# Performance work log

Hardware: AMD Instinct MI355X
Metric: run time of the kernel (lower is better)

The kernel has to match this reference:

```python
import jax, jax.numpy as jnp
from jax import lax
import numpy as np

B, T, H, W = 8, 32, 128, 128
D_MODEL, D_STATE, D_CONV, EXPAND = 256, 16, 4, 2
D_INNER = EXPAND * D_MODEL
DT_RANK = 16  # ceil(d_model/16)
CHANS = [3, 32, 64, 96]
COV_SCALE = 0.01


def setup_inputs() -> dict:
    key = jax.random.key(0)
    ks = iter(jax.random.split(key, 64))
    def n(shape, s=0.02):
        return jax.random.normal(next(ks), shape, dtype=jnp.float32) * s
    inp = {
        "frames": jax.random.normal(next(ks), (B, T, 3, H, W), dtype=jnp.float32),
        "target_bboxes": jax.random.uniform(next(ks), (B, T, 4), dtype=jnp.float32),
    }
    for i in range(3):
        inp[f"conv_w{i}"] = n((CHANS[i + 1], CHANS[i], 3, 3, 3))
        inp[f"conv_b{i}"] = jnp.zeros((CHANS[i + 1],), jnp.float32)
        inp[f"bn_g{i}"] = jnp.ones((CHANS[i + 1],), jnp.float32)
        inp[f"bn_b{i}"] = jnp.zeros((CHANS[i + 1],), jnp.float32)
    inp["ep_w"] = n((D_MODEL, CHANS[-1])); inp["ep_b"] = jnp.zeros((D_MODEL,), jnp.float32)
    inp["bp1_w"] = n((64, 4), 0.1); inp["bp1_b"] = jnp.zeros((64,), jnp.float32)
    inp["bp2_w"] = n((D_MODEL, 64)); inp["bp2_b"] = jnp.zeros((D_MODEL,), jnp.float32)
    inp["in_proj_w"] = n((2 * D_INNER, D_MODEL))
    inp["conv1d_w"] = n((D_INNER, 1, D_CONV), 0.1)
    inp["conv1d_b"] = jnp.zeros((D_INNER,), jnp.float32)
    inp["x_proj_w"] = n((DT_RANK + 2 * D_STATE, D_INNER))
    inp["dt_proj_w"] = n((D_INNER, DT_RANK), 0.1)
    inp["dt_proj_b"] = jnp.full((D_INNER,), -3.0, jnp.float32)
    inp["A_log"] = jnp.log(jnp.broadcast_to(jnp.arange(1, D_STATE + 1, dtype=jnp.float32), (D_INNER, D_STATE)))
    inp["D_param"] = jnp.ones((D_INNER,), jnp.float32)
    inp["out_proj_w"] = n((D_MODEL, D_INNER))
    inp["h1_w"] = n((D_MODEL // 2, D_MODEL)); inp["h1_b"] = jnp.zeros((D_MODEL // 2,), jnp.float32)
    inp["h2_w"] = n((4, D_MODEL // 2), 0.1); inp["h2_b"] = jnp.zeros((4,), jnp.float32)
    inp["kf_F"] = jnp.eye(4, dtype=jnp.float32) + n((4, 4), 0.01)
    inp["kf_H"] = jnp.eye(4, dtype=jnp.float32) + n((4, 4), 0.01)
    inp["kf_log_q"] = n((4,), 1.0) - 2.0
    inp["kf_log_r"] = n((4,), 1.0) - 2.0
    return inp


DN3D = ("NCDHW", "OIDHW", "NCDHW")


def _forward(frames, target_bboxes, conv_w0, conv_b0, bn_g0, bn_b0,
             conv_w1, conv_b1, bn_g1, bn_b1, conv_w2, conv_b2, bn_g2, bn_b2,
             ep_w, ep_b, bp1_w, bp1_b, bp2_w, bp2_b,
             in_proj_w, conv1d_w, conv1d_b, x_proj_w, dt_proj_w, dt_proj_b,
             A_log, D_param, out_proj_w, h1_w, h1_b, h2_w, h2_b,
             kf_F, kf_H, kf_log_q, kf_log_r):
    Bn, Tn = frames.shape[0], frames.shape[1]

    # ---- bbox_proj: Linear(4,64) -> ReLU -> Linear(64,d_model) ----
    bf = jax.nn.relu(target_bboxes @ bp1_w.T + bp1_b) @ bp2_w.T + bp2_b  # (B,T,Dm)

    # ---- 3D conv encoder (BN in eval mode: running stats 0/1 -> affine only) ----
    x = jnp.transpose(frames, (0, 2, 1, 3, 4))  # (B,C,T,H,W)
    for (w, b, g, be) in ((conv_w0, conv_b0, bn_g0, bn_b0),
                          (conv_w1, conv_b1, bn_g1, bn_b1),
                          (conv_w2, conv_b2, bn_g2, bn_b2)):
        x = lax.conv_general_dilated(x, w, (1, 2, 2), ((1, 1), (1, 1), (1, 1)),
                                     dimension_numbers=DN3D) + b[None, :, None, None, None]
        x = g[None, :, None, None, None] * x + be[None, :, None, None, None]
        x = jax.nn.relu(x)
        x = lax.reduce_window(x, -jnp.inf, lax.max, (1, 1, 1, 2, 2), (1, 1, 1, 2, 2), "VALID")
    x = x.mean(axis=(3, 4))                    # AdaptiveAvgPool3d((None,1,1)) -> (B,Cenc,T)
    ff = jnp.transpose(x, (0, 2, 1)) @ ep_w.T + ep_b  # (B,T,Dm)

    u = ff + bf

    # ---- Mamba block ----
    xz = u @ in_proj_w.T                        # (B,T,2*Di)
    xm, z = jnp.split(xz, 2, axis=-1)
    xc = jnp.transpose(xm, (0, 2, 1))           # (B,Di,T)
    xc = lax.conv_general_dilated(xc, conv1d_w, (1,), ((D_CONV - 1, 0),),
                                  dimension_numbers=("NCW", "OIW", "NCW"),
                                  feature_group_count=D_INNER) + conv1d_b[None, :, None]
    xs = jax.nn.silu(jnp.transpose(xc, (0, 2, 1)))  # (B,T,Di)
    xdbl = xs @ x_proj_w.T
    dt, Bm, Cm = jnp.split(xdbl, [DT_RANK, DT_RANK + D_STATE], axis=-1)
    dt = jax.nn.softplus(dt @ dt_proj_w.T + dt_proj_b)    # (B,T,Di)
    A = -jnp.exp(A_log)                                    # (Di,Ds)
    dA = jnp.exp(dt[..., None] * A)                        # (B,T,Di,Ds)
    dBx = dt[..., None] * Bm[:, :, None, :] * xs[..., None]

    def ssm_step(h, inputs):
        dA_t, dBx_t, C_t = inputs
        h = dA_t * h + dBx_t                               # (B,Di,Ds)
        y = jnp.einsum("bds,bs->bd", h, C_t)
        return h, y

    h0 = jnp.zeros((Bn, D_INNER, D_STATE), xs.dtype)
    _, ys = lax.scan(ssm_step, h0, (jnp.transpose(dA, (1, 0, 2, 3)),
                                    jnp.transpose(dBx, (1, 0, 2, 3)),
                                    jnp.transpose(Cm, (1, 0, 2))))
    y = jnp.transpose(ys, (1, 0, 2)) + D_param * xs
    y = y * jax.nn.silu(z)
    mo = y @ out_proj_w.T                                  # (B,T,Dm)

    # ---- measurement head ----
    meas = jax.nn.sigmoid(jax.nn.relu(mo @ h1_w.T + h1_b) @ h2_w.T + h2_b)  # (B,T,4)

    # ---- Kalman filter over T (scan) ----
    Q = jnp.diag(jnp.exp(kf_log_q) + 1e-6)
    R = jnp.diag(jnp.exp(kf_log_r) + 1e-6)
    I4 = jnp.eye(4, dtype=meas.dtype)
    Hb = jnp.broadcast_to(kf_H, (Bn, 4, 4))

    def kf_step(carry, m_t):
        s, P = carry
        s_pred = jnp.einsum("ij,bjk->bik", kf_F, s)
        P_pred = jnp.einsum("ij,bjk,lk->bil", kf_F, P, kf_F) + Q
        yres = m_t - jnp.einsum("ij,bjk->bik", kf_H, s_pred)
        S = jnp.einsum("ij,bjk,lk->bil", kf_H, P_pred, kf_H) + R
        SinvH = jnp.linalg.solve(S, Hb)                    # S^{-1} H
        K = jnp.einsum("bij,bkj->bik", P_pred, SinvH)      # P H^T S^{-T}
        s_new = s_pred + K @ yres
        IKH = I4 - K @ kf_H
        P_new = IKH @ P_pred @ jnp.swapaxes(IKH, -1, -2) + (K @ R) @ jnp.swapaxes(K, -1, -2)
        return (s_new, P_new), s_new[..., 0]

    state0 = target_bboxes[:, 0, :, None]                  # (B,4,1)
    cov0 = jnp.broadcast_to(I4 * COV_SCALE, (Bn, 4, 4))
    _, preds = lax.scan(kf_step, (state0, cov0), jnp.transpose(meas, (1, 0, 2))[..., None])
    kf_pred = jnp.transpose(preds, (1, 0, 2))              # (B,T,4)
    return kf_pred, meas


def reference(frames, target_bboxes, conv_w0, conv_b0, bn_g0, bn_b0,
              conv_w1, conv_b1, bn_g1, bn_b1, conv_w2, conv_b2, bn_g2, bn_b2,
              ep_w, ep_b, bp1_w, bp1_b, bp2_w, bp2_b,
              in_proj_w, conv1d_w, conv1d_b, x_proj_w, dt_proj_w, dt_proj_b,
              A_log, D_param, out_proj_w, h1_w, h1_b, h2_w, h2_b,
              kf_F, kf_H, kf_log_q, kf_log_r):
    return _forward(frames, target_bboxes, conv_w0, conv_b0, bn_g0, bn_b0,
                    conv_w1, conv_b1, bn_g1, bn_b1, conv_w2, conv_b2, bn_g2, bn_b2,
                    ep_w, ep_b, bp1_w, bp1_b, bp2_w, bp2_b,
                    in_proj_w, conv1d_w, conv1d_b, x_proj_w, dt_proj_w, dt_proj_b,
                    A_log, D_param, out_proj_w, h1_w, h1_b, h2_w, h2_b,
                    kf_F, kf_H, kf_log_q, kf_log_r)
```

## Files before the change

### kernel.cpp

```cpp
#include <hip/hip_runtime.h>
#include <math.h>

constexpr int Bn = 8, Tn = 32;
constexpr int D_INNER = 512;

typedef __attribute__((ext_vector_type(8))) short short8;
typedef __attribute__((ext_vector_type(8))) unsigned short ushort8;
typedef __attribute__((ext_vector_type(4))) float f32x4;

__device__ inline unsigned short f2bf(float x) {
    unsigned int u = __float_as_uint(x);
    unsigned int r = (u + 0x7FFF + ((u >> 16) & 1)) >> 16;
    return (unsigned short)r;
}

__global__ void prep_all(
    const float* __restrict__ cw0, const float* __restrict__ cw1,
    const float* __restrict__ cw2,
    const float* __restrict__ ip, const float* __restrict__ xp,
    const float* __restrict__ dt, const float* __restrict__ op,
    const float* __restrict__ h1, const float* __restrict__ h2,
    const float* __restrict__ ep, const float* __restrict__ bp2,
    const float* __restrict__ bp1,
    unsigned short* __restrict__ w0b, unsigned short* __restrict__ w1b,
    unsigned short* __restrict__ w2b, float* __restrict__ tW)
{
    int idx = blockIdx.x * blockDim.x + threadIdx.x;
    if (idx < 9216) {
        int d = idx;
        int sl = d & 7, sq = (d >> 3) & 3, co = (d >> 5) & 31;
        int r = d >> 10; int ky = r % 3, kt = r / 3;
        int q = sq ^ (co & 3) ^ ((co >> 2) & 3);
        float v = 0.f;
        if (q < 3 && sl < 3)
            v = cw0[((((size_t)co * 3 + sl) * 3 + kt) * 3 + ky) * 3 + q];
        w0b[d] = f2bf(v);
    } else if (idx < 64512) {
        int d = idx - 9216;
        int sl = d & 7, sg = (d >> 3) & 3, co = (d >> 5) & 63;
        int r = d >> 11; int k9 = r % 9, kt = r / 9;
        int ci = (sg ^ (co & 3)) * 8 + sl;
        w1b[d] = f2bf(cw1[((size_t)(co * 32 + ci) * 3 + kt) * 9 + k9]);
    } else if (idx < 230400) {
        int d = idx - 64512;
        int cip = d & 31; int rest = d >> 5;
        int co = rest % 96; rest /= 96;
        int k9 = rest % 9; int hh = rest / 9;
        int h = hh & 1, kt = hh >> 1;
        int ci = h * 32 + cip;
        w2b[d] = f2bf(cw2[((size_t)(co * 64 + ci) * 3 + kt) * 9 + k9]);
    } else if (idx < 730880) {
        int d = idx - 230400;
        const float* src; int N, K, base;
        if      (d < 262144) { src = ip;  N = 1024; K = 256; base = 0; }
        else if (d < 286720) { src = xp;  N = 48;   K = 512; base = 262144; }
        else if (d < 294912) { src = dt;  N = 512;  K = 16;  base = 286720; }
        else if (d < 425984) { src = op;  N = 256;  K = 512; base = 294912; }
        else if (d < 458752) { src = h1;  N = 128;  K = 256; base = 425984; }
        else if (d < 459264) { src = h2;  N = 4;    K = 128; base = 458752; }
        else if (d < 483840) { src = ep;  N = 256;  K = 96;  base = 459264; }
        else if (d < 500224) { src = bp2; N = 256;  K = 64;  base = 483840; }
        else                 { src = bp1; N = 64;   K = 4;   base = 500224; }
        int s = d - base;
        int o = s / K, k = s - o * K;
        tW[base + k * N + o] = src[s];
    }
}

constexpr int C0_STR  = 68;
constexpr int C0_BLKS = 17 * C0_STR;

__device__ inline void conv0_fill(unsigned short* dst, const float* __restrict__ in,
                                  int b, int ts, int yt, int xh, int tid)
{
    bool tok = (ts >= 0 && ts < Tn);
    const float* src = in + (size_t)(b * Tn + (tok ? ts : 0)) * 3 * 16384;
    for (int e = tid; e < C0_BLKS; e += 512) {
        int r = e / C0_STR, c = e - r * C0_STR;
        int gy = 16 * yt - 1 + r;
        int x  = 64 * xh + c - 1;
        bool ok = tok && gy >= 0 && gy < 128 && x >= 0 && x < 128;
        float v0 = 0.f, v1 = 0.f, v2 = 0.f;
        if (ok) {
            const float* p = src + gy * 128 + x;
            v0 = p[0]; v1 = p[16384]; v2 = p[32768];
        }
        ushort8 pk = (ushort8)0;
        pk[0] = f2bf(v0); pk[1] = f2bf(v1); pk[2] = f2bf(v2);
        *(ushort8*)(dst + (size_t)e * 8) = pk;
    }
}

__global__ __launch_bounds__(512) void conv0_kernel(
    const float* __restrict__ in, const unsigned short* __restrict__ w0b,
    const float* __restrict__ bias, const float* __restrict__ gam,
    const float* __restrict__ bet, unsigned short* __restrict__ out)
{
    int tid  = threadIdx.x;
    int lane = tid & 63;
    int wv   = __builtin_amdgcn_readfirstlane(tid >> 6);
    int q    = lane >> 4;
    int l15  = lane & 15;
    int pyp  = wv >> 1;
    int hx   = wv & 1;
    int bI = blockIdx.x;
    int bt = bI >> 4, yt = (bI >> 1) & 7, xh = bI & 1;
    int b = bt >> 5, t = bt & 31;

    __shared__ __align__(16) unsigned short S[C0_BLKS * 8];
    __shared__ __align__(16) unsigned short W[9 * 32 * 32];

    f32x4 acc[2][2];
    #pragma unroll
    for (int dy = 0; dy < 2; ++dy)
        #pragma unroll
        for (int nt = 0; nt < 2; ++nt) acc[dy][nt] = (f32x4)0.f;

    {
        const uint4* wsrc = (const uint4*)w0b;
        uint4* wdst = (uint4*)W;
        for (int e = tid; e < 1152; e += 512) wdst[e] = wsrc[e];
    }

    int oxl = hx * 16 + l15;

    for (int kt = 0; kt < 3; ++kt) {
        __syncthreads();
        conv0_fill(S, in, b, t + kt - 1, yt, xh, tid);
        __syncthreads();

        #pragma unroll
        for (int ky = 0; ky < 3; ++ky) {
            short8 bfr[2];
            #pragma unroll
            for (int nt = 0; nt < 2; ++nt) {
                int co = nt * 16 + l15;
                int i16 = ((kt * 3 + ky) * 32 + co) * 4 +
                          (q ^ (co & 3) ^ ((co >> 2) & 3));
                bfr[nt] = *(const short8*)(W + (size_t)i16 * 8);
            }
            #pragma unroll
            for (int dy = 0; dy < 2; ++dy) {
                int r = 4 * pyp + 2 * dy + ky;
                short8 af = (short8)0;
                if (q < 3)
                    af = *(const short8*)(S + (size_t)(r * C0_STR + 2 * oxl + q) * 8);
                #pragma unroll
                for (int nt = 0; nt < 2; ++nt)
                    acc[dy][nt] = __builtin_amdgcn_mfma_f32_16x16x32_bf16(
                        af, bfr[nt], acc[dy][nt], 0, 0, 0);
            }
        }
    }

    unsigned short* dst = out + (size_t)bt * 32768;
    #pragma unroll
    for (int nt = 0; nt < 2; ++nt) {
        int co = nt * 16 + l15;
        float bi = bias[co], g = gam[co], be = bet[co];
        #pragma unroll
        for (int j = 0; j < 2; ++j) {
            float m0 = fmaxf(fmaf(g, acc[0][nt][2 * j]     + bi, be), 0.f);
            float m1 = fmaxf(fmaf(g, acc[0][nt][2 * j + 1] + bi, be), 0.f);
            float m2 = fmaxf(fmaf(g, acc[1][nt][2 * j]     + bi, be), 0.f);
            float m3 = fmaxf(fmaf(g, acc[1][nt][2 * j + 1] + bi, be), 0.f);
            float p = fmaxf(fmaxf(m0, m1), fmaxf(m2, m3));
            int pox = xh * 16 + hx * 8 + q * 2 + j;
            int poy = yt * 4 + pyp;
            dst[(poy * 32 + pox) * 32 + co] = f2bf(p);
        }
    }
}

__global__ __launch_bounds__(512) void conv1_kernel(
    const unsigned short* __restrict__ in, const unsigned short* __restrict__ w1b,
    const float* __restrict__ bias, const float* __restrict__ gam,
    const float* __restrict__ bet, unsigned short* __restrict__ out)
{
    int tid  = threadIdx.x;
    int lane = tid & 63;
    int wv   = tid >> 6;
    int q    = lane >> 4;
    int l15  = lane & 15;
    int oyp  = wv >> 1;
    int nh   = wv & 1;
    int bt = blockIdx.x >> 1, half = blockIdx.x & 1;
    int b = bt >> 5, t = bt & 31;

    __shared__ __align__(16) unsigned short S[17 * 34 * 32];
    __shared__ __align__(16) unsigned short W[9 * 64 * 32];

    f32x4 acc[2][2];
    #pragma unroll
    for (int mt = 0; mt < 2; ++mt)
        #pragma unroll
        for (int nt = 0; nt < 2; ++nt) acc[mt][nt] = (f32x4)0.f;

    for (int kt = 0; kt < 3; ++kt) {
        int ts = t + kt - 1;
        if (ts < 0 || ts >= Tn) continue;
        __syncthreads();
        const unsigned short* src = in + (size_t)(b * Tn + ts) * 32768;
        for (int e = tid; e < 17 * 34 * 4; e += 512) {
            int sb = e & 3;
            int pos = e >> 2;
            int ys = pos / 34, xs = pos - ys * 34;
            int g = sb ^ ((xs >> 1) & 3);
            int y = 16 * half + ys - 1, x = xs - 1;
            ushort8 v = (ushort8)0;
            if (y >= 0 && x >= 0 && x < 32)
                v = *(const ushort8*)(src + ((y * 32 + x) * 32 + g * 8));
            *(ushort8*)(S + (size_t)e * 8) = v;
        }
        {
            const uint4* wsrc = (const uint4*)(w1b + kt * 18432);
            uint4* wdst = (uint4*)W;
            for (int e = tid; e < 2304; e += 512) wdst[e] = wsrc[e];
        }
        __syncthreads();

        for (int k9 = 0; k9 < 9; ++k9) {
            int ky = k9 / 3, kx = k9 - ky * 3;
            short8 bf[2];
            #pragma unroll
            for (int nt = 0; nt < 2; ++nt) {
                int co = nh * 32 + nt * 16 + l15;
                int blk = (k9 * 64 + co) * 4 + (q ^ (co & 3));
                bf[nt] = *(const short8*)(W + blk * 8);
            }
            short8 af[2];
            #pragma unroll
            for (int mt = 0; mt < 2; ++mt) {
                int oyl = 2 * oyp + mt;
                int ys = 2 * oyl + ky;
                int xs = 2 * l15 + kx;
                int blk = (ys * 34 + xs) * 4 + (q ^ ((xs >> 1) & 3));
                af[mt] = *(const short8*)(S + blk * 8);
            }
            #pragma unroll
            for (int mt = 0; mt < 2; ++mt)
                #pragma unroll
                for (int nt = 0; nt < 2; ++nt)
                    acc[mt][nt] = __builtin_amdgcn_mfma_f32_16x16x32_bf16(
                        af[mt], bf[nt], acc[mt][nt], 0, 0, 0);
        }
    }

    unsigned short* dst = out + (size_t)bt * 4096;
    #pragma unroll
    for (int nt = 0; nt < 2; ++nt) {
        int co = nh * 32 + nt * 16 + l15;
        float bi = bias[co], g = gam[co], be = bet[co];
        #pragma unroll
        for (int j = 0; j < 2; ++j) {
            float m0 = fmaxf(fmaf(g, acc[0][nt][2 * j]     + bi, be), 0.f);
            float m1 = fmaxf(fmaf(g, acc[0][nt][2 * j + 1] + bi, be), 0.f);
            float m2 = fmaxf(fmaf(g, acc[1][nt][2 * j]     + bi, be), 0.f);
            float m3 = fmaxf(fmaf(g, acc[1][nt][2 * j + 1] + bi, be), 0.f);
            float p = fmaxf(fmaxf(m0, m1), fmaxf(m2, m3));
            int px = 2 * q + j, py = half * 4 + oyp;
            dst[(py * 8 + px) * 64 + co] = f2bf(p);
        }
    }
}

__global__ __launch_bounds__(384) void conv2_kernel(
    const unsigned short* __restrict__ in, const unsigned short* __restrict__ w2b,
    const float* __restrict__ bias, const float* __restrict__ gam,
    const float* __restrict__ bet, float* __restrict__ out)
{
    int tid  = threadIdx.x;
    int lane = tid & 63;
    int wv   = tid >> 6;
    int q    = lane >> 4;
    int l15  = lane & 15;
    int bt = blockIdx.x;
    int b = bt >> 5, t = bt & 31;

    __shared__ __align__(16) unsigned short W[864 * 5 * 8];
    __shared__ __align__(16) unsigned short S[81 * 5 * 8];

    f32x4 acc = (f32x4)0.f;

    for (int kt = 0; kt < 3; ++kt) {
        int ts = t + kt - 1;
        if (ts < 0 || ts >= Tn) continue;
        for (int h = 0; h < 2; ++h) {
            __syncthreads();
            const unsigned short* wsrc = w2b + (size_t)((kt * 2 + h) * 9) * 96 * 32;
            for (int e = tid; e < 3456; e += 384) {
                int r = e >> 2, qq = e & 3;
                uint4 v = *(const uint4*)(wsrc + r * 32 + qq * 8);
                *(uint4*)(W + (r * 5 + qq) * 8) = v;
            }
            const unsigned short* src = in + (size_t)(b * Tn + ts) * 4096 + h * 32;
            for (int e = tid; e < 81 * 4; e += 384) {
                int cb = e & 3, p = e >> 2;
                int ys = p / 9, xs = p - ys * 9;
                int y = ys - 1, x = xs - 1;
                ushort8 v = (ushort8)0;
                if (y >= 0 && x >= 0 && y < 8 && x < 8)
                    v = *(const ushort8*)(src + ((y * 8 + x) * 64 + cb * 8));
                *(ushort8*)(S + (size_t)(p * 5 + cb) * 8) = v;
            }
            __syncthreads();

            int oy = l15 >> 2, ox = l15 & 3;
            #pragma unroll
            for (int k9 = 0; k9 < 9; ++k9) {
                int ky = k9 / 3, kx = k9 - ky * 3;
                short8 bf = *(const short8*)(W + (size_t)((k9 * 96 + wv * 16 + l15) * 5 + q) * 8);
                int p = (2 * oy + ky) * 9 + (2 * ox + kx);
                short8 af = *(const short8*)(S + (size_t)(p * 5 + q) * 8);
                acc = __builtin_amdgcn_mfma_f32_16x16x32_bf16(af, bf, acc, 0, 0, 0);
            }
        }
    }

    int co = wv * 16 + l15;
    float bi = bias[co], g = gam[co], be = bet[co];
    float v0 = fmaxf(fmaf(g, acc[0] + bi, be), 0.f);
    float v1 = fmaxf(fmaf(g, acc[1] + bi, be), 0.f);
    float v2 = fmaxf(fmaf(g, acc[2] + bi, be), 0.f);
    float v3 = fmaxf(fmaf(g, acc[3] + bi, be), 0.f);
    float p0 = fmaxf(v0, v1);
    float p1 = fmaxf(v2, v3);
    float r0 = fmaxf(p0, __shfl_xor(p0, 16));
    float r1 = fmaxf(p1, __shfl_xor(p1, 16));
    if ((q & 1) == 0) {
        int py = q >> 1;
        float* o = out + (size_t)(bt * 96 + co) * 4 + py * 2;
        o[0] = r0;
        o[1] = r1;
    }
}

__global__ __launch_bounds__(256) void fuse_u_inproj(
    const float* __restrict__ buf2, const float* __restrict__ epT,
    const float* __restrict__ ep_b, const float* __restrict__ bb,
    const float* __restrict__ bp1T, const float* __restrict__ bp1_b,
    const float* __restrict__ bp2T, const float* __restrict__ bp2_b,
    const float* __restrict__ ipwT, float* __restrict__ xzb)
{
    int bt = blockIdx.x;
    int m  = threadIdx.x;
    __shared__ float hs[64];
    __shared__ float gap[96];
    __shared__ float u_lds[256];
    if (m < 64) {
        float a = bp1_b[m];
        #pragma unroll
        for (int k = 0; k < 4; ++k) a = fmaf(bp1T[k * 64 + m], bb[bt * 4 + k], a);
        hs[m] = fmaxf(a, 0.f);
    } else if (m < 160) {
        int c = m - 64;
        const float* p = buf2 + ((size_t)bt * 96 + c) * 4;
        gap[c] = 0.25f * (p[0] + p[1] + p[2] + p[3]);
    }
    __syncthreads();
    float ff = ep_b[m];
    for (int c = 0; c < 96; ++c) ff = fmaf(gap[c], epT[c * 256 + m], ff);
    float bfv = bp2_b[m];
    for (int j = 0; j < 64; ++j) bfv = fmaf(hs[j], bp2T[j * 256 + m], bfv);
    u_lds[m] = ff + bfv;
    __syncthreads();

    const float4* wbase = (const float4*)ipwT + m;
    float4 acc = {0.f, 0.f, 0.f, 0.f};
    for (int k = 0; k < 256; ++k) {
        float uk = u_lds[k];
        float4 w4 = wbase[(size_t)k * 256];
        acc.x = fmaf(uk, w4.x, acc.x);
        acc.y = fmaf(uk, w4.y, acc.y);
        acc.z = fmaf(uk, w4.z, acc.z);
        acc.w = fmaf(uk, w4.w, acc.w);
    }
    *(float4*)(xzb + (size_t)bt * 1024 + 4 * m) = acc;
}

__global__ __launch_bounds__(512) void convxd_kernel(
    const float* __restrict__ xzb, const float* __restrict__ c1w,
    const float* __restrict__ c1b, const float* __restrict__ xpw,
    const float* __restrict__ dtwT, const float* __restrict__ dt_b,
    float* __restrict__ xsb, float* __restrict__ xdb, float* __restrict__ dtbf)
{
    int bt = blockIdx.x;
    int b = bt >> 5, t = bt & 31;
    int tid = threadIdx.x;
    __shared__ float xs_lds[512];
    __shared__ float xd_lds[48];

    {
        float acc = c1b[tid];
        #pragma unroll
        for (int k = 0; k < 4; ++k) {
            int ts = t - 3 + k;
            if (ts >= 0)
                acc = fmaf(c1w[tid * 4 + k], xzb[(size_t)(b * Tn + ts) * 1024 + tid], acc);
        }
        float v = acc / (1.f + expf(-acc));
        xs_lds[tid] = v;
        xsb[(size_t)bt * 512 + tid] = v;
    }
    __syncthreads();

    {
        int wv = tid >> 6, ln = tid & 63;
        #pragma unroll
        for (int u = 0; u < 6; ++u) {
            int o = wv * 6 + u;
            const float* wrow = xpw + (size_t)o * 512;
            float acc = 0.f;
            #pragma unroll
            for (int e = 0; e < 8; ++e)
                acc = fmaf(wrow[ln + 64 * e], xs_lds[ln + 64 * e], acc);
            acc += __shfl_xor(acc, 32); acc += __shfl_xor(acc, 16);
            acc += __shfl_xor(acc, 8);  acc += __shfl_xor(acc, 4);
            acc += __shfl_xor(acc, 2);  acc += __shfl_xor(acc, 1);
            if (ln == 0) {
                xd_lds[o] = acc;
                xdb[(size_t)bt * 48 + o] = acc;
            }
        }
    }
    __syncthreads();

    {
        float a = dt_b[tid];
        #pragma unroll
        for (int k = 0; k < 16; ++k) a = fmaf(xd_lds[k], dtwT[k * 512 + tid], a);
        a = (a > 20.f) ? a : log1pf(expf(a));
        dtbf[(size_t)bt * 512 + tid] = a;
    }
}

__global__ __launch_bounds__(256) void ssm_kernel(
    const float* __restrict__ xdbl, const float* __restrict__ dtb,
    const float* __restrict__ xs, const float* __restrict__ xz,
    const float* __restrict__ A_log, const float* __restrict__ Dp,
    float* __restrict__ y)
{
    int tid = threadIdx.x;
    int lane = tid & 63;
    int s = lane & 15, dsub = lane >> 4;
    int gid = blockIdx.x * 4 + (tid >> 6);
    int b = gid >> 7;
    int d = ((gid & 127) << 2) + dsub;

    float A = -expf(A_log[d * 16 + s]);
    float Dv = Dp[d];
    float h = 0.f;
    for (int t = 0; t < Tn; ++t) {
        int bt = b * Tn + t;
        float dtv = dtb[(size_t)bt * 512 + d];
        float xv  = xs [(size_t)bt * 512 + d];
        float Bs  = xdbl[(size_t)bt * 48 + 16 + s];
        float Cs  = xdbl[(size_t)bt * 48 + 32 + s];
        float dA = expf(dtv * A);
        h = fmaf(dA, h, dtv * Bs * xv);
        float c = h * Cs;
        c += __shfl_xor(c, 8, 16);
        c += __shfl_xor(c, 4, 16);
        c += __shfl_xor(c, 2, 16);
        c += __shfl_xor(c, 1, 16);
        if (s == 0) {
            float zv = xz[(size_t)bt * 1024 + 512 + d];
            float sig = 1.f / (1.f + expf(-zv));
            y[(size_t)bt * 512 + d] = (c + Dv * xv) * (zv * sig);
        }
    }
}

__global__ __launch_bounds__(256) void out_head_kernel(
    const float* __restrict__ yb, const float* __restrict__ opwT,
    const float* __restrict__ h1wT, const float* __restrict__ h1_b,
    const float* __restrict__ h2w, const float* __restrict__ h2_b,
    float* __restrict__ meas_out)
{
    int bt = blockIdx.x;
    int m  = threadIdx.x;
    __shared__ float y_lds[512];
    __shared__ float mo_lds[256];
    __shared__ float hid_lds[128];

    y_lds[m]       = yb[(size_t)bt * 512 + m];
    y_lds[m + 256] = yb[(size_t)bt * 512 + m + 256];
    __syncthreads();

    {
        float a = 0.f;
        for (int k = 0; k < 512; ++k) a = fmaf(y_lds[k], opwT[k * 256 + m], a);
        mo_lds[m] = a;
    }
    __syncthreads();

    if (m < 128) {
        float a = h1_b[m];
        for (int k = 0; k < 256; ++k) a = fmaf(mo_lds[k], h1wT[k * 128 + m], a);
        hid_lds[m] = fmaxf(a, 0.f);
    }
    __syncthreads();

    if (m < 64) {
        int o2 = m >> 4, l15 = m & 15;
        float acc = 0.f;
        #pragma unroll
        for (int e = 0; e < 8; ++e)
            acc = fmaf(h2w[o2 * 128 + l15 + 16 * e], hid_lds[l15 + 16 * e], acc);
        acc += __shfl_xor(acc, 8, 16);
        acc += __shfl_xor(acc, 4, 16);
        acc += __shfl_xor(acc, 2, 16);
        acc += __shfl_xor(acc, 1, 16);
        if (l15 == 0) {
            float a = acc + h2_b[o2];
            meas_out[bt * 4 + o2] = 1.f / (1.f + expf(-a));
        }
    }
}

__device__ __forceinline__ float kf_mm(float Av, float Bv, int i, int j, int gb) {
    float c = 0.f;
    #pragma unroll
    for (int k = 0; k < 4; ++k)
        c = fmaf(__shfl(Av, gb + i * 4 + k, 64), __shfl(Bv, gb + k * 4 + j, 64), c);
    return c;
}
__device__ __forceinline__ float kf_mmT(float Av, float Bv, int i, int j, int gb) {
    float c = 0.f;
    #pragma unroll
    for (int k = 0; k < 4; ++k)
        c = fmaf(__shfl(Av, gb + i * 4 + k, 64), __shfl(Bv, gb + j * 4 + k, 64), c);
    return c;
}

__global__ __launch_bounds__(128) void kf_kernel(
    const float* __restrict__ meas, const float* __restrict__ bb,
    const float* __restrict__ Fin, const float* __restrict__ Hmin,
    const float* __restrict__ lq, const float* __restrict__ lr,
    float* __restrict__ pred)
{
    int tid = threadIdx.x;
    int b   = tid >> 4;
    int l16 = tid & 15;
    int i = l16 >> 2, j = l16 & 3;
    int gb = tid & 48;

    float Fv = Fin[l16], Hv = Hmin[l16];
    float R4[4];
    #pragma unroll
    for (int k = 0; k < 4; ++k) R4[k] = expf(lr[k]) + 1e-6f;
    float qi = expf(lq[i]) + 1e-6f;

    float sv = bb[b * 128 + j];
    float Pv = (i == j) ? 0.01f : 0.f;

    for (int t = 0; t < Tn; ++t) {
        float mv = meas[(b * Tn + t) * 4 + j];
        float tr = Fv * sv;
        tr += __shfl_xor(tr, 1); tr += __shfl_xor(tr, 2);
        float spv = tr;
        float spj = __shfl(spv, gb + j * 4, 64);
        float FPv = kf_mm(Fv, Pv, i, j, gb);
        float Ppv = kf_mmT(FPv, Fv, i, j, gb) + ((i == j) ? qi : 0.f);
        float hsp = Hv * spj;
        hsp += __shfl_xor(hsp, 1); hsp += __shfl_xor(hsp, 2);
        float yrv = mv - __shfl(hsp, gb + j * 4, 64);
        float HPv = kf_mm(Hv, Ppv, i, j, gb);
        float Sv = kf_mmT(HPv, Hv, i, j, gb) + ((i == j) ? R4[i] : 0.f);
        float Xv = Hv;
        #pragma unroll
        for (int c = 0; c < 4; ++c) {
            float piv = __shfl(Sv, gb + c * 5, 64);
            float dinv = 1.f / piv;
            if (i == c) { Sv *= dinv; Xv *= dinv; }
            float Scj = __shfl(Sv, gb + c * 4 + j, 64);
            float Xcj = __shfl(Xv, gb + c * 4 + j, 64);
            float f = __shfl(Sv, gb + i * 4 + c, 64);
            if (i != c) { Sv = fmaf(-f, Scj, Sv); Xv = fmaf(-f, Xcj, Xv); }
        }
        float Kv = kf_mmT(Ppv, Xv, i, j, gb);
        float t3 = Kv * yrv;
        t3 += __shfl_xor(t3, 1); t3 += __shfl_xor(t3, 2);
        float snv = spv + t3;
        if (j == 0) pred[(b * Tn + t) * 4 + i] = snv;
        float IKHv = ((i == j) ? 1.f : 0.f) - kf_mm(Kv, Hv, i, j, gb);
        float T1v = kf_mm(IKHv, Ppv, i, j, gb);
        float krk = 0.f;
        #pragma unroll
        for (int k = 0; k < 4; ++k)
            krk = fmaf(__shfl(Kv, gb + i * 4 + k, 64) * R4[k],
                       __shfl(Kv, gb + j * 4 + k, 64), krk);
        Pv = kf_mmT(T1v, IKHv, i, j, gb) + krk;
        sv = __shfl(snv, gb + j * 4, 64);
    }
}

extern "C" void kernel_launch(void* const* d_in, const int* in_sizes, int n_in,
                              void* d_out, int out_size, void* d_ws, size_t ws_size,
                              hipStream_t stream)
{
    const float* frames = (const float*)d_in[0];
    const float* bb     = (const float*)d_in[1];
    const float* cw0 = (const float*)d_in[2],  *cb0 = (const float*)d_in[3];
    const float* g0  = (const float*)d_in[4],  *be0 = (const float*)d_in[5];
    const float* cw1 = (const float*)d_in[6],  *cb1 = (const float*)d_in[7];
    const float* g1  = (const float*)d_in[8],  *be1 = (const float*)d_in[9];
    const float* cw2 = (const float*)d_in[10], *cb2 = (const float*)d_in[11];
    const float* g2  = (const float*)d_in[12], *be2 = (const float*)d_in[13];
    const float* ep_w  = (const float*)d_in[14], *ep_b  = (const float*)d_in[15];
    const float* bp1_w = (const float*)d_in[16], *bp1_b = (const float*)d_in[17];
    const float* bp2_w = (const float*)d_in[18], *bp2_b = (const float*)d_in[19];
    const float* in_proj_w = (const float*)d_in[20];
    const float* c1w = (const float*)d_in[21], *c1b = (const float*)d_in[22];
    const float* x_proj_w = (const float*)d_in[23];
    const float* dt_w = (const float*)d_in[24], *dt_b = (const float*)d_in[25];
    const float* A_log = (const float*)d_in[26], *Dp = (const float*)d_in[27];
    const float* out_proj_w = (const float*)d_in[28];
    const float* h1_w = (const float*)d_in[29], *h1_b = (const float*)d_in[30];
    const float* h2_w = (const float*)d_in[31], *h2_b = (const float*)d_in[32];
    const float* kfF = (const float*)d_in[33], *kfH = (const float*)d_in[34];
    const float* kfq = (const float*)d_in[35], *kfr = (const float*)d_in[36];

    float* ws   = (float*)d_ws;
    float* buf2 = ws;
    float* xzb  = buf2 + 98304;
    float* xsb  = xzb  + 262144;
    float* xdb  = xsb  + 131072;
    float* dtbf = xdb  + 12288;
    float* yb   = dtbf + 131072;
    float* tW   = yb   + 131072;
    unsigned short* buf0b = (unsigned short*)(tW + 500480);
    unsigned short* buf1b = buf0b + 8388608;
    unsigned short* w2b   = buf1b + 131072;
    unsigned short* w1b   = w2b + 165888;
    unsigned short* w0b   = w1b + 55296;

    float* ipwT = tW;
    float* dtwT = tW + 286720;
    float* opwT = tW + 294912;
    float* h1wT = tW + 425984;
    float* epwT = tW + 459264;
    float* bp2T = tW + 483840;
    float* bp1T = tW + 500224;

    float* kf_out   = (float*)d_out;
    float* meas_out = kf_out + Bn * Tn * 4;

    auto nblk = [](int n) { return dim3((unsigned)((n + 255) / 256)); };

    prep_all<<<nblk(730880), 256, 0, stream>>>(cw0, cw1, cw2,
                                               in_proj_w, x_proj_w, dt_w, out_proj_w,
                                               h1_w, h2_w, ep_w, bp2_w, bp1_w,
                                               w0b, w1b, w2b, tW);

    conv0_kernel<<<dim3(4096), 512, 0, stream>>>(frames, w0b, cb0, g0, be0, buf0b);
    conv1_kernel<<<dim3(512), 512, 0, stream>>>(buf0b, w1b, cb1, g1, be1, buf1b);
    conv2_kernel<<<dim3(256), 384, 0, stream>>>(buf1b, w2b, cb2, g2, be2, buf2);

    fuse_u_inproj<<<dim3(256), 256, 0, stream>>>(buf2, epwT, ep_b, bb, bp1T, bp1_b,
                                                 bp2T, bp2_b, ipwT, xzb);
    convxd_kernel<<<dim3(256), 512, 0, stream>>>(xzb, c1w, c1b, x_proj_w,
                                                 dtwT, dt_b, xsb, xdb, dtbf);
    ssm_kernel<<<dim3(256), 256, 0, stream>>>(xdb, dtbf, xsb, xzb, A_log, Dp, yb);
    out_head_kernel<<<dim3(256), 256, 0, stream>>>(yb, opwT, h1wT, h1_b,
                                                   h2_w, h2_b, meas_out);
    kf_kernel<<<dim3(1), 128, 0, stream>>>(meas_out, bb, kfF, kfH, kfq, kfr, kf_out);
}
```

Before: 331.2 us.

## Reuse conv0 input frames across four output timesteps per block

```diff
diff --git a/kernel.cpp b/kernel.cpp
--- a/kernel.cpp
+++ b/kernel.cpp
@@ -85,11 +85,40 @@
             const float* p = src + gy * 128 + x;
             v0 = p[0]; v1 = p[16384]; v2 = p[32768];
         }
-        ushort8 pk = (ushort8)0;
-        pk[0] = f2bf(v0); pk[1] = f2bf(v1); pk[2] = f2bf(v2);
-        *(ushort8*)(dst + (size_t)e * 8) = pk;
-    }
-}
+        unsigned int w0, w1;
+        asm("v_cvt_pk_bf16_f32 %0, %1, %2" : "=v"(w0) : "v"(v0), "v"(v1));
+        asm("v_cvt_pk_bf16_f32 %0, %1, %2" : "=v"(w1) : "v"(v2), "v"(0.f));
+        uint4 pk; pk.x = w0; pk.y = w1; pk.z = 0u; pk.w = 0u;
+        *(uint4*)(dst + (size_t)e * 8) = pk;
+    }
+}
+
+#define C0_S1(KA, AA)                                   \
+  { _Pragma("unroll")                                   \
+    for (int ky = 0; ky < 3; ++ky) {                    \
+      short8 af[2]; ldA(ky, af);                        \
+      short8 bf[2];                                     \
+      ldB(KA, ky, bf); mm(af, bf, AA);                  \
+    } }
+
+#define C0_S2(KA, AA, KB, AB)                           \
+  { _Pragma("unroll")                                   \
+    for (int ky = 0; ky < 3; ++ky) {                    \
+      short8 af[2]; ldA(ky, af);                        \
+      short8 bf[2];                                     \
+      ldB(KA, ky, bf); mm(af, bf, AA);                  \
+      ldB(KB, ky, bf); mm(af, bf, AB);                  \
+    } }
+
+#define C0_S3(KA, AA, KB, AB, KC, AC)                   \
+  { _Pragma("unroll")                                   \
+    for (int ky = 0; ky < 3; ++ky) {                    \
+      short8 af[2]; ldA(ky, af);                        \
+      short8 bf[2];                                     \
+      ldB(KA, ky, bf); mm(af, bf, AA);                  \
+      ldB(KB, ky, bf); mm(af, bf, AB);                  \
+      ldB(KC, ky, bf); mm(af, bf, AC);                  \
+    } }
 
 __global__ __launch_bounds__(512) void conv0_kernel(
     const float* __restrict__ in, const unsigned short* __restrict__ w0b,
@@ -104,17 +133,22 @@
     int pyp  = wv >> 1;
     int hx   = wv & 1;
     int bI = blockIdx.x;
-    int bt = bI >> 4, yt = (bI >> 1) & 7, xh = bI & 1;
-    int b = bt >> 5, t = bt & 31;
+    int sp = bI & 15;
+    int yt = sp >> 1, xh = sp & 1;
+    int btc = bI >> 4;
+    int b = btc >> 3, tc = btc & 7;
+    int t0 = tc * 4;
 
     __shared__ __align__(16) unsigned short S[C0_BLKS * 8];
     __shared__ __align__(16) unsigned short W[9 * 32 * 32];
 
-    f32x4 acc[2][2];
+    f32x4 A0[2][2], A1[2][2], A2[2][2];
     #pragma unroll
     for (int dy = 0; dy < 2; ++dy)
         #pragma unroll
-        for (int nt = 0; nt < 2; ++nt) acc[dy][nt] = (f32x4)0.f;
+        for (int nt = 0; nt < 2; ++nt) {
+            A0[dy][nt] = (f32x4)0.f; A1[dy][nt] = (f32x4)0.f; A2[dy][nt] = (f32x4)0.f;
+        }
 
     {
         const uint4* wsrc = (const uint4*)w0b;
@@ -124,52 +158,93 @@
 
     int oxl = hx * 16 + l15;
 
-    for (int kt = 0; kt < 3; ++kt) {
-        __syncthreads();
-        conv0_fill(S, in, b, t + kt - 1, yt, xh, tid);
-        __syncthreads();
-
-        #pragma unroll
-        for (int ky = 0; ky < 3; ++ky) {
-            short8 bfr[2];
+    float biv[2] = {bias[l15], bias[l15 + 16]};
+    float gv [2] = {gam [l15], gam [l15 + 16]};
+    float bev[2] = {bet [l15], bet [l15 + 16]};
+
+    auto ldA = [&](int ky, short8 (&af)[2]) {
+        #pragma unroll
+        for (int dy = 0; dy < 2; ++dy) {
+            int r = 4 * pyp + 2 * dy + ky;
+            short8 a = (short8)0;
+            if (q < 3)
+                a = *(const short8*)(S + (size_t)(r * C0_STR + 2 * oxl + q) * 8);
+            af[dy] = a;
+        }
+    };
+    auto ldB = [&](int kt, int ky, short8 (&bf)[2]) {
+        #pragma unroll
+        for (int nt = 0; nt < 2; ++nt) {
+            int co = nt * 16 + l15;
+            int i16 = ((kt * 3 + ky) * 32 + co) * 4 +
+                      (q ^ (co & 3) ^ ((co >> 2) & 3));
+            bf[nt] = *(const short8*)(W + (size_t)i16 * 8);
+        }
+    };
+    auto mm = [&](short8 (&af)[2], short8 (&bf)[2], f32x4 (&A)[2][2]) {
+        #pragma unroll
+        for (int dy = 0; dy < 2; ++dy)
             #pragma unroll
-            for (int nt = 0; nt < 2; ++nt) {
-                int co = nt * 16 + l15;
-                int i16 = ((kt * 3 + ky) * 32 + co) * 4 +
-                          (q ^ (co & 3) ^ ((co >> 2) & 3));
-                bfr[nt] = *(const short8*)(W + (size_t)i16 * 8);
+            for (int nt = 0; nt < 2; ++nt)
+                A[dy][nt] = __builtin_amdgcn_mfma_f32_16x16x32_bf16(
+                    af[dy], bf[nt], A[dy][nt], 0, 0, 0);
+    };
+    auto flush = [&](f32x4 (&A)[2][2], int t_out) {
+        unsigned short* dst = out + (size_t)(b * Tn + t_out) * 32768;
+        #pragma unroll
+        for (int nt = 0; nt < 2; ++nt) {
+            int co = nt * 16 + l15;
+            float bi = biv[nt], g = gv[nt], be = bev[nt];
+            #pragma unroll
+            for (int j = 0; j < 2; ++j) {
+                float m0 = fmaxf(fmaf(g, A[0][nt][2 * j]     + bi, be), 0.f);
+                float m1 = fmaxf(fmaf(g, A[0][nt][2 * j + 1] + bi, be), 0.f);
+                float m2 = fmaxf(fmaf(g, A[1][nt][2 * j]     + bi, be), 0.f);
+                float m3 = fmaxf(fmaf(g, A[1][nt][2 * j + 1] + bi, be), 0.f);
+                float p = fmaxf(fmaxf(m0, m1), fmaxf(m2, m3));
+                int pox = xh * 16 + hx * 8 + q * 2 + j;
+                int poy = yt * 4 + pyp;
+                dst[(poy * 32 + pox) * 32 + co] = f2bf(p);
             }
+        }
+        #pragma unroll
+        for (int dy = 0; dy < 2; ++dy)
             #pragma unroll
-            for (int dy = 0; dy < 2; ++dy) {
-                int r = 4 * pyp + 2 * dy + ky;
-                short8 af = (short8)0;
-                if (q < 3)
-                    af = *(const short8*)(S + (size_t)(r * C0_STR + 2 * oxl + q) * 8);
-                #pragma unroll
-                for (int nt = 0; nt < 2; ++nt)
-                    acc[dy][nt] = __builtin_amdgcn_mfma_f32_16x16x32_bf16(
-                        af, bfr[nt], acc[dy][nt], 0, 0, 0);
-            }
-        }
-    }
-
-    unsigned short* dst = out + (size_t)bt * 32768;
-    #pragma unroll
-    for (int nt = 0; nt < 2; ++nt) {
-        int co = nt * 16 + l15;
-        float bi = bias[co], g = gam[co], be = bet[co];
-        #pragma unroll
-        for (int j = 0; j < 2; ++j) {
-            float m0 = fmaxf(fmaf(g, acc[0][nt][2 * j]     + bi, be), 0.f);
-            float m1 = fmaxf(fmaf(g, acc[0][nt][2 * j + 1] + bi, be), 0.f);
-            float m2 = fmaxf(fmaf(g, acc[1][nt][2 * j]     + bi, be), 0.f);
-            float m3 = fmaxf(fmaf(g, acc[1][nt][2 * j + 1] + bi, be), 0.f);
-            float p = fmaxf(fmaxf(m0, m1), fmaxf(m2, m3));
-            int pox = xh * 16 + hx * 8 + q * 2 + j;
-            int poy = yt * 4 + pyp;
-            dst[(poy * 32 + pox) * 32 + co] = f2bf(p);
-        }
-    }
+            for (int nt = 0; nt < 2; ++nt) A[dy][nt] = (f32x4)0.f;
+    };
+
+    conv0_fill(S, in, b, t0 - 1, yt, xh, tid);
+    __syncthreads();
+    C0_S1(0, A0);
+
+    __syncthreads();
+    conv0_fill(S, in, b, t0, yt, xh, tid);
+    __syncthreads();
+    C0_S2(1, A0, 0, A1);
+
+    __syncthreads();
+    conv0_fill(S, in, b, t0 + 1, yt, xh, tid);
+    __syncthreads();
+    C0_S3(2, A0, 1, A1, 0, A2);
+    flush(A0, t0);
+
+    __syncthreads();
+    conv0_fill(S, in, b, t0 + 2, yt, xh, tid);
+    __syncthreads();
+    C0_S3(0, A0, 2, A1, 1, A2);
+    flush(A1, t0 + 1);
+
+    __syncthreads();
+    conv0_fill(S, in, b, t0 + 3, yt, xh, tid);
+    __syncthreads();
+    C0_S2(1, A0, 2, A2);
+    flush(A2, t0 + 2);
+
+    __syncthreads();
+    conv0_fill(S, in, b, t0 + 4, yt, xh, tid);
+    __syncthreads();
+    C0_S1(2, A0);
+    flush(A0, t0 + 3);
 }
 
 __global__ __launch_bounds__(512) void conv1_kernel(
@@ -653,7 +728,7 @@
                                                h1_w, h2_w, ep_w, bp2_w, bp1_w,
                                                w0b, w1b, w2b, tW);
 
-    conv0_kernel<<<dim3(4096), 512, 0, stream>>>(frames, w0b, cb0, g0, be0, buf0b);
+    conv0_kernel<<<dim3(1024), 512, 0, stream>>>(frames, w0b, cb0, g0, be0, buf0b);
     conv1_kernel<<<dim3(512), 512, 0, stream>>>(buf0b, w1b, cb1, g1, be1, buf1b);
     conv2_kernel<<<dim3(256), 384, 0, stream>>>(buf1b, w2b, cb2, g2, be2, buf2);
 
```

New measurement: 326.1 us. About the same (-1.5%).

## Precompute Kalman gains in prep kernel and software-pipeline conv0 frame loads

Applied to the files above, without the earlier changes.

```diff
diff --git a/kernel.cpp b/kernel.cpp
--- a/kernel.cpp
+++ b/kernel.cpp
@@ -12,6 +12,21 @@
     unsigned int u = __float_as_uint(x);
     unsigned int r = (u + 0x7FFF + ((u >> 16) & 1)) >> 16;
     return (unsigned short)r;
+}
+
+__device__ __forceinline__ float kf_mm(float Av, float Bv, int i, int j, int gb) {
+    float c = 0.f;
+    #pragma unroll
+    for (int k = 0; k < 4; ++k)
+        c = fmaf(__shfl(Av, gb + i * 4 + k, 64), __shfl(Bv, gb + k * 4 + j, 64), c);
+    return c;
+}
+__device__ __forceinline__ float kf_mmT(float Av, float Bv, int i, int j, int gb) {
+    float c = 0.f;
+    #pragma unroll
+    for (int k = 0; k < 4; ++k)
+        c = fmaf(__shfl(Av, gb + i * 4 + k, 64), __shfl(Bv, gb + j * 4 + k, 64), c);
+    return c;
 }
 
 __global__ void prep_all(
@@ -22,8 +37,11 @@
     const float* __restrict__ h1, const float* __restrict__ h2,
     const float* __restrict__ ep, const float* __restrict__ bp2,
     const float* __restrict__ bp1,
+    const float* __restrict__ kfF, const float* __restrict__ kfH,
+    const float* __restrict__ lq, const float* __restrict__ lr,
     unsigned short* __restrict__ w0b, unsigned short* __restrict__ w1b,
-    unsigned short* __restrict__ w2b, float* __restrict__ tW)
+    unsigned short* __restrict__ w2b, float* __restrict__ tW,
+    float* __restrict__ kfK)
 {
     int idx = blockIdx.x * blockDim.x + threadIdx.x;
     if (idx < 9216) {
@@ -64,32 +82,49 @@
         int s = d - base;
         int o = s / K, k = s - o * K;
         tW[base + k * N + o] = src[s];
+    } else {
+        if (threadIdx.x >= 64) return;
+        int l16 = threadIdx.x & 15;
+        int i = l16 >> 2, j = l16 & 3;
+        int gb = threadIdx.x & 48;
+        float Fv = kfF[l16], Hv = kfH[l16];
+        float R4[4];
+        #pragma unroll
+        for (int k = 0; k < 4; ++k) R4[k] = expf(lr[k]) + 1e-6f;
+        float qi = expf(lq[i]) + 1e-6f;
+        float Pv = (i == j) ? 0.01f : 0.f;
+        for (int t = 0; t < Tn; ++t) {
+            float FPv = kf_mm(Fv, Pv, i, j, gb);
+            float Ppv = kf_mmT(FPv, Fv, i, j, gb) + ((i == j) ? qi : 0.f);
+            float HPv = kf_mm(Hv, Ppv, i, j, gb);
+            float Sv = kf_mmT(HPv, Hv, i, j, gb) + ((i == j) ? R4[i] : 0.f);
+            float Xv = Hv;
+            #pragma unroll
+            for (int c = 0; c < 4; ++c) {
+                float piv = __shfl(Sv, gb + c * 5, 64);
+                float dinv = 1.f / piv;
+                if (i == c) { Sv *= dinv; Xv *= dinv; }
+                float Scj = __shfl(Sv, gb + c * 4 + j, 64);
+                float Xcj = __shfl(Xv, gb + c * 4 + j, 64);
+                float f = __shfl(Sv, gb + i * 4 + c, 64);
+                if (i != c) { Sv = fmaf(-f, Scj, Sv); Xv = fmaf(-f, Xcj, Xv); }
+            }
+            float Kv = kf_mmT(Ppv, Xv, i, j, gb);
+            if (threadIdx.x < 16) kfK[t * 16 + l16] = Kv;
+            float IKHv = ((i == j) ? 1.f : 0.f) - kf_mm(Kv, Hv, i, j, gb);
+            float T1v = kf_mm(IKHv, Ppv, i, j, gb);
+            float krk = 0.f;
+            #pragma unroll
+            for (int k = 0; k < 4; ++k)
+                krk = fmaf(__shfl(Kv, gb + i * 4 + k, 64) * R4[k],
+                           __shfl(Kv, gb + j * 4 + k, 64), krk);
+            Pv = kf_mmT(T1v, IKHv, i, j, gb) + krk;
+        }
     }
 }
 
 constexpr int C0_STR  = 68;
 constexpr int C0_BLKS = 17 * C0_STR;
-
-__device__ inline void conv0_fill(unsigned short* dst, const float* __restrict__ in,
-                                  int b, int ts, int yt, int xh, int tid)
-{
-    bool tok = (ts >= 0 && ts < Tn);
-    const float* src = in + (size_t)(b * Tn + (tok ? ts : 0)) * 3 * 16384;
-    for (int e = tid; e < C0_BLKS; e += 512) {
-        int r = e / C0_STR, c = e - r * C0_STR;
-        int gy = 16 * yt - 1 + r;
-        int x  = 64 * xh + c - 1;
-        bool ok = tok && gy >= 0 && gy < 128 && x >= 0 && x < 128;
-        float v0 = 0.f, v1 = 0.f, v2 = 0.f;
-        if (ok) {
-            const float* p = src + gy * 128 + x;
-            v0 = p[0]; v1 = p[16384]; v2 = p[32768];
-        }
-        ushort8 pk = (ushort8)0;
-        pk[0] = f2bf(v0); pk[1] = f2bf(v1); pk[2] = f2bf(v2);
-        *(ushort8*)(dst + (size_t)e * 8) = pk;
-    }
-}
 
 __global__ __launch_bounds__(512) void conv0_kernel(
     const float* __restrict__ in, const unsigned short* __restrict__ w0b,
@@ -124,11 +159,48 @@
 
     int oxl = hx * 16 + l15;
 
-    for (int kt = 0; kt < 3; ++kt) {
-        __syncthreads();
-        conv0_fill(S, in, b, t + kt - 1, yt, xh, tid);
-        __syncthreads();
-
+    int offs[3]; bool oksp[3];
+    #pragma unroll
+    for (int i = 0; i < 3; ++i) {
+        int e = tid + 512 * i;
+        int r = e / C0_STR, c = e - r * C0_STR;
+        int gy = 16 * yt - 1 + r;
+        int x  = 64 * xh + c - 1;
+        bool act = (e < C0_BLKS);
+        oksp[i] = act && gy >= 0 && gy < 128 && x >= 0 && x < 128;
+        offs[i] = gy * 128 + x;
+    }
+
+    float biv[2] = {bias[l15], bias[l15 + 16]};
+    float gv [2] = {gam [l15], gam [l15 + 16]};
+    float bev[2] = {bet [l15], bet [l15 + 16]};
+
+    float pf[3][3];
+    auto ldG = [&](int ts) {
+        bool tok = ((unsigned)ts < (unsigned)Tn);
+        const float* base = in + (size_t)(b * Tn + (tok ? ts : 0)) * 49152;
+        #pragma unroll
+        for (int i = 0; i < 3; ++i) {
+            bool ok = tok && oksp[i];
+            const float* p = base + offs[i];
+            pf[i][0] = ok ? p[0]     : 0.f;
+            pf[i][1] = ok ? p[16384] : 0.f;
+            pf[i][2] = ok ? p[32768] : 0.f;
+        }
+    };
+    auto stS = [&]() {
+        #pragma unroll
+        for (int i = 0; i < 3; ++i) {
+            if (i < 2 || tid < C0_BLKS - 1024) {
+                unsigned w0_, w1_;
+                asm("v_cvt_pk_bf16_f32 %0, %1, %2" : "=v"(w0_) : "v"(pf[i][0]), "v"(pf[i][1]));
+                asm("v_cvt_pk_bf16_f32 %0, %1, %2" : "=v"(w1_) : "v"(pf[i][2]), "v"(0.f));
+                uint4 pk; pk.x = w0_; pk.y = w1_; pk.z = 0u; pk.w = 0u;
+                *(uint4*)(S + (size_t)(tid + 512 * i) * 8) = pk;
+            }
+        }
+    };
+    auto compute = [&](int kt) {
         #pragma unroll
         for (int ky = 0; ky < 3; ++ky) {
             short8 bfr[2];
@@ -151,13 +223,28 @@
                         af, bfr[nt], acc[dy][nt], 0, 0, 0);
             }
         }
-    }
+    };
+
+    ldG(t - 1);
+    stS();
+    ldG(t);
+    __syncthreads();
+    compute(0);
+    __syncthreads();
+    stS();
+    ldG(t + 1);
+    __syncthreads();
+    compute(1);
+    __syncthreads();
+    stS();
+    __syncthreads();
+    compute(2);
 
     unsigned short* dst = out + (size_t)bt * 32768;
     #pragma unroll
     for (int nt = 0; nt < 2; ++nt) {
         int co = nt * 16 + l15;
-        float bi = bias[co], g = gam[co], be = bet[co];
+        float bi = biv[nt], g = gv[nt], be = bev[nt];
         #pragma unroll
         for (int j = 0; j < 2; ++j) {
             float m0 = fmaxf(fmaf(g, acc[0][nt][2 * j]     + bi, be), 0.f);
@@ -518,26 +605,10 @@
     }
 }
 
-__device__ __forceinline__ float kf_mm(float Av, float Bv, int i, int j, int gb) {
-    float c = 0.f;
-    #pragma unroll
-    for (int k = 0; k < 4; ++k)
-        c = fmaf(__shfl(Av, gb + i * 4 + k, 64), __shfl(Bv, gb + k * 4 + j, 64), c);
-    return c;
-}
-__device__ __forceinline__ float kf_mmT(float Av, float Bv, int i, int j, int gb) {
-    float c = 0.f;
-    #pragma unroll
-    for (int k = 0; k < 4; ++k)
-        c = fmaf(__shfl(Av, gb + i * 4 + k, 64), __shfl(Bv, gb + j * 4 + k, 64), c);
-    return c;
-}
-
 __global__ __launch_bounds__(128) void kf_kernel(
     const float* __restrict__ meas, const float* __restrict__ bb,
     const float* __restrict__ Fin, const float* __restrict__ Hmin,
-    const float* __restrict__ lq, const float* __restrict__ lr,
-    float* __restrict__ pred)
+    const float* __restrict__ kfK, float* __restrict__ pred)
 {
     int tid = threadIdx.x;
     int b   = tid >> 4;
@@ -546,51 +617,22 @@
     int gb = tid & 48;
 
     float Fv = Fin[l16], Hv = Hmin[l16];
-    float R4[4];
-    #pragma unroll
-    for (int k = 0; k < 4; ++k) R4[k] = expf(lr[k]) + 1e-6f;
-    float qi = expf(lq[i]) + 1e-6f;
-
     float sv = bb[b * 128 + j];
-    float Pv = (i == j) ? 0.01f : 0.f;
 
     for (int t = 0; t < Tn; ++t) {
         float mv = meas[(b * Tn + t) * 4 + j];
+        float Kv = kfK[t * 16 + l16];
         float tr = Fv * sv;
         tr += __shfl_xor(tr, 1); tr += __shfl_xor(tr, 2);
         float spv = tr;
         float spj = __shfl(spv, gb + j * 4, 64);
-        float FPv = kf_mm(Fv, Pv, i, j, gb);
-        float Ppv = kf_mmT(FPv, Fv, i, j, gb) + ((i == j) ? qi : 0.f);
         float hsp = Hv * spj;
         hsp += __shfl_xor(hsp, 1); hsp += __shfl_xor(hsp, 2);
         float yrv = mv - __shfl(hsp, gb + j * 4, 64);
-        float HPv = kf_mm(Hv, Ppv, i, j, gb);
-        float Sv = kf_mmT(HPv, Hv, i, j, gb) + ((i == j) ? R4[i] : 0.f);
-        float Xv = Hv;
-        #pragma unroll
-        for (int c = 0; c < 4; ++c) {
-            float piv = __shfl(Sv, gb + c * 5, 64);
-            float dinv = 1.f / piv;
-            if (i == c) { Sv *= dinv; Xv *= dinv; }
-            float Scj = __shfl(Sv, gb + c * 4 + j, 64);
-            float Xcj = __shfl(Xv, gb + c * 4 + j, 64);
-            float f = __shfl(Sv, gb + i * 4 + c, 64);
-            if (i != c) { Sv = fmaf(-f, Scj, Sv); Xv = fmaf(-f, Xcj, Xv); }
-        }
-        float Kv = kf_mmT(Ppv, Xv, i, j, gb);
         float t3 = Kv * yrv;
         t3 += __shfl_xor(t3, 1); t3 += __shfl_xor(t3, 2);
         float snv = spv + t3;
         if (j == 0) pred[(b * Tn + t) * 4 + i] = snv;
-        float IKHv = ((i == j) ? 1.f : 0.f) - kf_mm(Kv, Hv, i, j, gb);
-        float T1v = kf_mm(IKHv, Ppv, i, j, gb);
-        float krk = 0.f;
-        #pragma unroll
-        for (int k = 0; k < 4; ++k)
-            krk = fmaf(__shfl(Kv, gb + i * 4 + k, 64) * R4[k],
-                       __shfl(Kv, gb + j * 4 + k, 64), krk);
-        Pv = kf_mmT(T1v, IKHv, i, j, gb) + krk;
         sv = __shfl(snv, gb + j * 4, 64);
     }
 }
@@ -629,7 +671,8 @@
     float* dtbf = xdb  + 12288;
     float* yb   = dtbf + 131072;
     float* tW   = yb   + 131072;
-    unsigned short* buf0b = (unsigned short*)(tW + 500480);
+    float* kfK  = tW + 500480;
+    unsigned short* buf0b = (unsigned short*)(kfK + 512);
     unsigned short* buf1b = buf0b + 8388608;
     unsigned short* w2b   = buf1b + 131072;
     unsigned short* w1b   = w2b + 165888;
@@ -646,12 +689,11 @@
     float* kf_out   = (float*)d_out;
     float* meas_out = kf_out + Bn * Tn * 4;
 
-    auto nblk = [](int n) { return dim3((unsigned)((n + 255) / 256)); };
-
-    prep_all<<<nblk(730880), 256, 0, stream>>>(cw0, cw1, cw2,
-                                               in_proj_w, x_proj_w, dt_w, out_proj_w,
-                                               h1_w, h2_w, ep_w, bp2_w, bp1_w,
-                                               w0b, w1b, w2b, tW);
+    prep_all<<<dim3(2856), 256, 0, stream>>>(cw0, cw1, cw2,
+                                             in_proj_w, x_proj_w, dt_w, out_proj_w,
+                                             h1_w, h2_w, ep_w, bp2_w, bp1_w,
+                                             kfF, kfH, kfq, kfr,
+                                             w0b, w1b, w2b, tW, kfK);
 
     conv0_kernel<<<dim3(4096), 512, 0, stream>>>(frames, w0b, cb0, g0, be0, buf0b);
     conv1_kernel<<<dim3(512), 512, 0, stream>>>(buf0b, w1b, cb1, g1, be1, buf1b);
@@ -664,5 +706,5 @@
     ssm_kernel<<<dim3(256), 256, 0, stream>>>(xdb, dtbf, xsb, xzb, A_log, Dp, yb);
     out_head_kernel<<<dim3(256), 256, 0, stream>>>(yb, opwT, h1wT, h1_b,
                                                    h2_w, h2_b, meas_out);
-    kf_kernel<<<dim3(1), 128, 0, stream>>>(meas_out, bb, kfF, kfH, kfq, kfr, kf_out);
-}
+    kf_kernel<<<dim3(1), 128, 0, stream>>>(meas_out, bb, kfF, kfH, kfK, kf_out);
+}
```

Result: no change. 326.3 us (-1.5%).
